# Kernel optimization log

Hardware: AMD Instinct MI355X
Metric: run time of the kernel (lower is better)

Reference implementation:

```python
import jax, jax.numpy as jnp
import numpy as np

EPS = 1e-6


def _expand_mask(mask, D, H, W):
    # mask: (B,1,f,f,f) bool -> (B,1,D,H,W) via repeat_interleave on each spatial axis
    m = jnp.repeat(mask, D // mask.shape[2], axis=2)
    m = jnp.repeat(m, H // mask.shape[3], axis=3)
    m = jnp.repeat(m, W // mask.shape[4], axis=4)
    return m


def setup_inputs() -> dict:
    key = jax.random.key(0)
    ks = jax.random.split(key, 10)
    B, C, D, H, W = 2, 192, 32, 32, 32
    K, HID = 7, 4 * C
    x = jax.random.normal(ks[0], (B, C, D, H, W), dtype=jnp.float32)
    mask = jax.random.randint(ks[1], (B, 1, 8, 8, 8), 0, 2) > 0
    dw_w = jax.random.normal(ks[2], (C, 1, K, K, K), dtype=jnp.float32) * (1.0 / np.sqrt(K**3))
    dw_b = jnp.zeros((C,), dtype=jnp.float32)
    ln_w = jnp.ones((C,), dtype=jnp.float32)
    ln_b = jnp.zeros((C,), dtype=jnp.float32)
    w1 = jax.random.normal(ks[3], (C, HID), dtype=jnp.float32) * (1.0 / np.sqrt(C))
    b1 = jnp.zeros((HID,), dtype=jnp.float32)
    w2 = jax.random.normal(ks[4], (HID, C), dtype=jnp.float32) * (1.0 / np.sqrt(HID))
    b2 = jnp.zeros((C,), dtype=jnp.float32)
    gamma = jnp.full((C,), 1e-6, dtype=jnp.float32)
    return {"x": x, "mask": mask, "dw_w": dw_w, "dw_b": dw_b, "ln_w": ln_w,
            "ln_b": ln_b, "w1": w1, "b1": b1, "w2": w2, "b2": b2, "gamma": gamma}


def reference(x, mask, dw_w, dw_b, ln_w, ln_b, w1, b1, w2, b2, gamma):
    B, C, D, H, W = x.shape
    m = _expand_mask(mask, D, H, W)              # (B,1,D,H,W) bool
    mf = m.astype(x.dtype)

    # depthwise 3D conv, SAME padding (padding = kernel//2), groups = C
    y = jax.lax.conv_general_dilated(
        x, dw_w, window_strides=(1, 1, 1), padding='SAME',
        dimension_numbers=('NCDHW', 'OIDHW', 'NCDHW'),
        feature_group_count=C)
    y = y + dw_b[None, :, None, None, None]

    # channels_last: (B,D,H,W,C)
    y = jnp.transpose(y, (0, 2, 3, 4, 1))

    # sparse LayerNorm over channel dim: normalize all tokens, keep only active
    # (equivalent to gather->LN->scatter-into-zeros in the original)
    mu = jnp.mean(y, axis=-1, keepdims=True)
    var = jnp.mean(jnp.square(y - mu), axis=-1, keepdims=True)
    ln = (y - mu) * jax.lax.rsqrt(var + EPS) * ln_w + ln_b
    ln = ln * jnp.transpose(mf, (0, 2, 3, 4, 1))  # zero inactive tokens

    # pointwise MLP
    h = jax.nn.gelu(jnp.einsum('bdhwc,ce->bdhwe', ln, w1) + b1, approximate=False)
    o = jnp.einsum('bdhwe,ec->bdhwc', h, w2) + b2
    o = gamma * o

    # back to channels_first and final sparse mask
    o = jnp.transpose(o, (0, 4, 1, 2, 3)) * mf
    return o
```

## Files before the change

kernel.cpp:

```cpp
#include <hip/hip_runtime.h>
#include <hip/hip_bf16.h>

typedef __attribute__((ext_vector_type(2))) float f2v;
typedef __attribute__((ext_vector_type(4))) float f4v;
typedef __attribute__((ext_vector_type(8))) short bf8v;
typedef __attribute__((ext_vector_type(8))) _Float16 h8v;

#define NPOS 32768
#define CCH  192
#define HID  768

#define WS_Y    ((size_t)0)
#define WS_B1F  ((size_t)25165824)
#define WS_B2F  ((size_t)25460736)
#define WS_WPF  ((size_t)25755648)
#define WS_B3F  ((size_t)26056704)
#define WS_TOTAL_MFMA ((size_t)35690496)
#define WS_TOTAL_DOT2 ((size_t)26056704)

__device__ inline unsigned short f2bf(float f){
  unsigned int u = __float_as_uint(f);
  u += 0x7FFFu + ((u >> 16) & 1u);
  return (unsigned short)(u >> 16);
}
__device__ inline float bf2f(unsigned short s){
  return __uint_as_float(((unsigned int)s) << 16);
}
__device__ inline float gelu_f(float x){
  float u = 0.7978845608028654f * x * fmaf(0.044715f, x*x, 1.0f);
  float e = __expf(2.0f*u);
  float th = __fdividef(e - 1.0f, e + 1.0f);
  return 0.5f*x*(1.0f + th);
}

#define DOT2(A, X, W) \
  asm("v_dot2_f32_f16 %0, %1, %2, %0" : "+v"(A) : "v"(X), "s"(W))

#define ZSTR 712
__global__ __launch_bounds__(256) void conv_mfma_kernel(
    const float* __restrict__ x, const float* __restrict__ dw_b,
    const unsigned short* __restrict__ b3f, unsigned short* __restrict__ yc)
{
  __shared__ unsigned short tile[22*ZSTR];

  int bid = blockIdx.x;
  int c = bid % 192;
  int r = bid / 192;
  int xq = r & 1, yq = (r >> 1) & 1, zh = (r >> 2) & 1, b = r >> 3;
  int tx0 = xq*16, ty0 = yq*16, zb = zh*16;

  int tid = threadIdx.x;
  const float* xsrc = x + ((size_t)(b*CCH + c))*NPOS;

  #pragma unroll
  for (int it = 0; it < 8; ++it) {
    int idx = tid + 256*it;
    if (idx < 1936) {
      int ci = idx & 3;
      int row = idx >> 2;
      int lz = row / 22, ly = row - lz*22;
      int gz = zb - 3 + lz, gy = ty0 - 3 + ly;
      f4v v0 = {0.f,0.f,0.f,0.f}, v1 = {0.f,0.f,0.f,0.f};
      if (((unsigned)gz < 32u) & ((unsigned)gy < 32u) & (ci < 3)) {
        int gx0 = tx0 - 4 + 8*ci;
        const float* src = xsrc + (size_t)gz*1024 + gy*32;
        if ((unsigned)gx0 <= 28u)     v0 = *(const f4v*)(src + gx0);
        if ((unsigned)(gx0+4) <= 28u) v1 = *(const f4v*)(src + gx0 + 4);
      }
      h8v pk;
      pk[0] = (_Float16)v0[0]; pk[1] = (_Float16)v0[1];
      pk[2] = (_Float16)v0[2]; pk[3] = (_Float16)v0[3];
      pk[4] = (_Float16)v1[0]; pk[5] = (_Float16)v1[1];
      pk[6] = (_Float16)v1[2]; pk[7] = (_Float16)v1[3];
      *(h8v*)(tile + lz*ZSTR + ly*32 + ci*8) = pk;
    }
  }
  __syncthreads();

  int wv = tid >> 6, lane = tid & 63;
  int q = lane >> 4, zm = lane & 15;

  const unsigned short* abase = tile + (size_t)zm*ZSTR + q*8;
  const unsigned short* bbase = b3f + ((size_t)c*49)*512 + (size_t)lane*8;

  f4v acc[4];
  #pragma unroll
  for (int t = 0; t < 4; ++t) acc[t] = (f4v){0.f,0.f,0.f,0.f};

  h8v Bc = *(const h8v*)(bbase);
  #pragma unroll 1
  for (int kz = 0; kz < 7; ++kz) {
    h8v Af[10];
    #pragma unroll
    for (int rr = 0; rr < 10; ++rr)
      Af[rr] = *(const h8v*)(abase + kz*ZSTR + (4*wv + rr)*32);
    #pragma unroll
    for (int ky = 0; ky < 7; ++ky) {
      int tap = kz*7 + ky;
      int tnx = (tap < 48) ? tap + 1 : 48;
      h8v Bn = *(const h8v*)(bbase + (size_t)tnx*512);
      acc[0] = __builtin_amdgcn_mfma_f32_16x16x32_f16(Af[ky+0], Bc, acc[0], 0, 0, 0);
      acc[1] = __builtin_amdgcn_mfma_f32_16x16x32_f16(Af[ky+1], Bc, acc[1], 0, 0, 0);
      acc[2] = __builtin_amdgcn_mfma_f32_16x16x32_f16(Af[ky+2], Bc, acc[2], 0, 0, 0);
      acc[3] = __builtin_amdgcn_mfma_f32_16x16x32_f16(Af[ky+3], Bc, acc[3], 0, 0, 0);
      Bc = Bn;
    }
  }

  float bias = dw_b[c];
  int cz = zh*4 + q;
  int cx = (tx0 >> 2) + (zm >> 2);
  int xr = zm & 3;
  int cy = (ty0 >> 2) + wv;
  int cell = cz*64 + cy*8 + cx;
  unsigned short* yb0 = yc + (((size_t)(b*512 + cell))*192 + c)*64 + xr;
  #pragma unroll
  for (int t = 0; t < 4; ++t) {
    unsigned short* yb = yb0 + t*4;
    yb[0]  = f2bf(acc[t][0] + bias);
    yb[16] = f2bf(acc[t][1] + bias);
    yb[32] = f2bf(acc[t][2] + bias);
    yb[48] = f2bf(acc[t][3] + bias);
  }
}

__global__ __launch_bounds__(256, 6) void conv_dw_f16_kernel(
    const float* __restrict__ x, const float* __restrict__ dw_b,
    const unsigned int* __restrict__ wpf, unsigned short* __restrict__ yc)
{
  __shared__ unsigned short ring[22*528];

  int bid = blockIdx.x;
  int c = bid % 192;
  int r = bid / 192;
  int xq = r & 1, yq = (r >> 1) & 1, zh = (r >> 2) & 1, b = r >> 3;
  int tx0 = xq*16, ty0 = yq*16, zb = zh*16;

  int tid = threadIdx.x;
  const float* xsrc = x + ((size_t)(b*CCH + c))*NPOS;

  for (int idx = tid; idx < 2904; idx += 256) {
    int sl = idx / 132;
    int rem = idx - sl*132;
    int rr = rem / 6, ci = rem - rr*6;
    int zi = zb - 3 + sl, gy = ty0 - 3 + rr, gx = tx0 - 4 + 4*ci;
    f4v v = {0.f, 0.f, 0.f, 0.f};
    if ((unsigned)zi < 32u && (unsigned)gy < 32u && (unsigned)gx <= 28u)
      v = *(const f4v*)(xsrc + (size_t)zi*1024 + gy*32 + gx);
    union { _Float16 h[4]; uint2 u2; } pk;
    pk.h[0] = (_Float16)v[0]; pk.h[1] = (_Float16)v[1];
    pk.h[2] = (_Float16)v[2]; pk.h[3] = (_Float16)v[3];
    *(uint2*)(ring + sl*528 + rr*24 + ci*4) = pk.u2;
  }
  __syncthreads();

  int p = tid & 15, zl = tid >> 4;
  int px = p & 3, py = p >> 2;
  int y0 = py*4, px4 = px*4;
  const unsigned short* base = ring + zl*528 + y0*24 + px4;
  const unsigned int* wb = wpf + (size_t)c*392;

  float acc[4][4];
  #pragma unroll
  for (int i = 0; i < 4; ++i)
    #pragma unroll
    for (int j = 0; j < 4; ++j) acc[i][j] = 0.f;

  #pragma unroll 1
  for (int s = 0; s < 7; ++s) {
    const unsigned short* sb = base + s*528;
    const unsigned int* wrow = wb + s*56;
    #pragma unroll
    for (int rr = 0; rr < 10; ++rr) {
      const unsigned short* rb = sb + rr*24;
      uint2 q0 = *(const uint2*)(rb);
      uint2 q1 = *(const uint2*)(rb + 4);
      uint2 q2 = *(const uint2*)(rb + 8);
      unsigned int D[6] = {q0.x, q0.y, q1.x, q1.y, q2.x, q2.y};
      #pragma unroll
      for (int dy = 0; dy < 4; ++dy) {
        int ky = rr - dy;
        if (ky < 0 || ky > 6) continue;
        const unsigned int* wk = wrow + ky*8;
        #pragma unroll
        for (int t = 0; t < 4; ++t) {
          DOT2(acc[dy][0], D[t],   wk[t]);
          DOT2(acc[dy][1], D[t+1], wk[4+t]);
          DOT2(acc[dy][2], D[t+1], wk[t]);
          DOT2(acc[dy][3], D[t+2], wk[4+t]);
        }
      }
    }
  }

  float bias = dw_b[c];
  int z = zb + zl;
  int cz = z >> 2, cx = (tx0 >> 2) + px, cy = (ty0 >> 2) + py;
  int cell = cz*64 + cy*8 + cx;
  unsigned short* ybase = yc + (((size_t)(b*512 + cell))*192 + c)*64;
  int tokz = (z & 3)*16;
  #pragma unroll
  for (int dy = 0; dy < 4; ++dy) {
    ushort4 o;
    o.x = f2bf(acc[dy][0] + bias);
    o.y = f2bf(acc[dy][1] + bias);
    o.z = f2bf(acc[dy][2] + bias);
    o.w = f2bf(acc[dy][3] + bias);
    *(ushort4*)(ybase + tokz + dy*4) = o;
  }
}

__global__ __launch_bounds__(256) void conv_dw_f32_kernel(
    const float* __restrict__ x, const float* __restrict__ dw_w,
    const float* __restrict__ dw_b, unsigned short* __restrict__ yc)
{
  __shared__ float ring[22*528];

  int bid = blockIdx.x;
  int c = bid % 192;
  int r = bid / 192;
  int xq = r & 1, yq = (r >> 1) & 1, zh = (r >> 2) & 1, b = r >> 3;
  int tx0 = xq*16, ty0 = yq*16, zb = zh*16;

  int tid = threadIdx.x;
  const float* xsrc = x + ((size_t)(b*CCH + c))*NPOS;

  for (int idx = tid; idx < 2904; idx += 256) {
    int sl = idx / 132;
    int rem = idx - sl*132;
    int rr = rem / 6, ci = rem - rr*6;
    int zi = zb - 3 + sl, gy = ty0 - 3 + rr, gx = tx0 - 4 + 4*ci;
    f4v v = {0.f, 0.f, 0.f, 0.f};
    if ((unsigned)zi < 32u && (unsigned)gy < 32u && (unsigned)gx <= 28u)
      v = *(const f4v*)(xsrc + (size_t)zi*1024 + gy*32 + gx);
    *(f4v*)(ring + sl*528 + rr*24 + ci*4) = v;
  }
  __syncthreads();

  int p = tid & 15, zl = tid >> 4;
  int px = p & 3, py = p >> 2;
  int y0 = py*4, px4 = px*4;
  const float* base = ring + zl*528 + y0*24 + px4;
  const float* wbase = dw_w + (size_t)c*343;

  f2v acc[8];
  #pragma unroll
  for (int i = 0; i < 8; ++i) acc[i] = (f2v){0.f, 0.f};

  #pragma unroll 1
  for (int s = 0; s < 7; ++s) {
    const float* sb = base + s*528;
    f4v n0 = *(const f4v*)(sb);
    f4v n1 = *(const f4v*)(sb + 4);
    f4v n2 = *(const f4v*)(sb + 8);
    #pragma unroll
    for (int rr = 0; rr < 10; ++rr) {
      f4v r0 = n0, r1 = n1, r2 = n2;
      if (rr < 9) {
        n0 = *(const f4v*)(sb + (rr+1)*24);
        n1 = *(const f4v*)(sb + (rr+1)*24 + 4);
        n2 = *(const f4v*)(sb + (rr+1)*24 + 8);
      }
      f2v pr[10];
      pr[1] = (f2v){r0[1], r0[2]};
      pr[2] = (f2v){r0[2], r0[3]};
      pr[3] = (f2v){r0[3], r1[0]};
      pr[4] = (f2v){r1[0], r1[1]};
      pr[5] = (f2v){r1[1], r1[2]};
      pr[6] = (f2v){r1[2], r1[3]};
      pr[7] = (f2v){r1[3], r2[0]};
      pr[8] = (f2v){r2[0], r2[1]};
      pr[9] = (f2v){r2[1], r2[2]};
      #pragma unroll
      for (int dy = 0; dy < 4; ++dy) {
        int ky = rr - dy;
        if (ky < 0 || ky > 6) continue;
        #pragma unroll
        for (int kx = 0; kx < 7; ++kx) {
          float w = wbase[s*49 + ky*7 + kx];
          f2v wv = (f2v){w, w};
          acc[dy*2+0] = __builtin_elementwise_fma(wv, pr[kx+1], acc[dy*2+0]);
          acc[dy*2+1] = __builtin_elementwise_fma(wv, pr[kx+3], acc[dy*2+1]);
        }
      }
    }
  }

  float bias = dw_b[c];
  int z = zb + zl;
  int cz = z >> 2, cx = (tx0 >> 2) + px, cy = (ty0 >> 2) + py;
  int cell = cz*64 + cy*8 + cx;
  unsigned short* ybase = yc + (((size_t)(b*512 + cell))*192 + c)*64;
  int tokz = (z & 3)*16;
  #pragma unroll
  for (int dy = 0; dy < 4; ++dy) {
    ushort4 o;
    o.x = f2bf(acc[dy*2+0][0] + bias);
    o.y = f2bf(acc[dy*2+0][1] + bias);
    o.z = f2bf(acc[dy*2+1][0] + bias);
    o.w = f2bf(acc[dy*2+1][1] + bias);
    *(ushort4*)(ybase + tokz + dy*4) = o;
  }
}

__global__ __launch_bounds__(256) void prep_w_kernel(
    const float* __restrict__ w1, const float* __restrict__ w2,
    const float* __restrict__ dw_w,
    unsigned short* __restrict__ b1f, unsigned short* __restrict__ b2f,
    unsigned int* __restrict__ wpf, unsigned short* __restrict__ b3f)
{
  int gid = blockIdx.x*256 + threadIdx.x;
  if (gid < 18432) {
    int fi = gid;
    int lane = fi & 63, fr = fi >> 6;
    int nt = fr / 6, ks = fr - nt*6;
    int n  = nt*16 + (lane & 15);
    int kb = ks*32 + (lane >> 4)*8;
    #pragma unroll
    for (int j = 0; j < 8; ++j) b1f[fi*8 + j] = f2bf(w1[(kb+j)*HID + n]);
  } else if (gid < 36864) {
    int fi = gid - 18432;
    int lane = fi & 63, fr = fi >> 6;
    int nt = fr / 24, ks = fr - nt*24;
    int n  = nt*16 + (lane & 15);
    int kb = ks*32 + (lane >> 4)*8;
    #pragma unroll
    for (int j = 0; j < 8; ++j) b2f[fi*8 + j] = f2bf(w2[(kb+j)*CCH + n]);
  } else if (gid < 46272) {
    int ci = gid - 36864;
    int cch = ci / 49, t7 = ci - cch*49;
    const float* wr = dw_w + cch*343 + t7*7;
    float w[8];
    #pragma unroll
    for (int j = 0; j < 7; ++j) w[j] = wr[j];
    w[7] = 0.f;
    union { _Float16 h[2]; unsigned int u; } pk;
    #pragma unroll
    for (int t = 0; t < 4; ++t) {
      pk.h[0] = (t == 0) ? (_Float16)0.f : (_Float16)w[2*t-1];
      pk.h[1] = (_Float16)w[2*t];
      wpf[ci*8 + t] = pk.u;
    }
    #pragma unroll
    for (int t = 0; t < 4; ++t) {
      pk.h[0] = (_Float16)w[2*t];
      pk.h[1] = (_Float16)w[2*t+1];
      wpf[ci*8 + 4 + t] = pk.u;
    }
  } else if (gid < 648384) {
    int fi = gid - 46272;
    int lane = fi & 63, frag = fi >> 6;
    int cch = frag / 49, tap = frag - cch*49;
    const float* wr = dw_w + cch*343 + tap*7;
    int q = lane >> 4, n = lane & 15;
    h8v pk;
    #pragma unroll
    for (int j = 0; j < 8; ++j) {
      int t = q*8 + j - n - 1;
      pk[j] = (t >= 0 && t <= 6) ? (_Float16)wr[t] : (_Float16)0.f;
    }
    *(h8v*)(b3f + (size_t)fi*8) = pk;
  }
}

__global__ __launch_bounds__(256) void mlp_kernel(
    const unsigned short* __restrict__ yc, const unsigned short* __restrict__ b1f,
    const unsigned short* __restrict__ b2f, const float* __restrict__ b1,
    const float* __restrict__ b2, const float* __restrict__ gamma,
    const float* __restrict__ ln_w, const float* __restrict__ ln_b,
    const int* __restrict__ mask, float* __restrict__ out)
{
  int bid = blockIdx.x;
  int b = bid >> 9, cell = bid & 511;
  int cz = cell >> 6, cy = (cell >> 3) & 7, cx = cell & 7;
  int z0 = cz*4, y0 = cy*4, x0 = cx*4;
  int tid = threadIdx.x, wave = tid >> 6, lane = tid & 63;
  int lq = lane >> 4, ln15 = lane & 15;

  if (mask[bid] == 0) {
    f4v z4 = {0.f, 0.f, 0.f, 0.f};
    #pragma unroll
    for (int pp = 0; pp < 12; ++pp) {
      int i4 = tid + 256*pp;
      int c = i4 >> 4, rem = i4 & 15;
      int dz = rem >> 2, dy = rem & 3;
      *(f4v*)(out + ((size_t)(b*CCH + c))*NPOS
                  + (size_t)(z0+dz)*1024 + (y0+dy)*32 + x0) = z4;
    }
    return;
  }

  __shared__ __align__(16) char uni[26112];
  unsigned short* ymat = (unsigned short*)uni;
  unsigned short* hbuf = (unsigned short*)uni;
  __shared__ unsigned short aFrag[12288];
  __shared__ float sred[2][4][64];
  __shared__ float murs[2][64];

  const unsigned short* ysrc = yc + (size_t)bid*12288;

  #pragma unroll
  for (int k = 0; k < 12; ++k) {
    int idx = tid + 256*k;
    int c = idx >> 4, t4 = idx & 15;
    *(ushort4*)(ymat + c*68 + t4*4) = *(const ushort4*)(ysrc + c*64 + t4*4);
  }
  __syncthreads();

  {
    int tok = tid & 63, part = tid >> 6;
    float S = 0.f, Q = 0.f;
    #pragma unroll
    for (int j = 0; j < 48; ++j) {
      float v = bf2f(ymat[(part*48 + j)*68 + tok]);
      S += v; Q = fmaf(v, v, Q);
    }
    sred[0][part][tok] = S; sred[1][part][tok] = Q;
  }
  __syncthreads();
  if (tid < 64) {
    float S = sred[0][0][tid] + sred[0][1][tid] + sred[0][2][tid] + sred[0][3][tid];
    float Q = sred[1][0][tid] + sred[1][1][tid] + sred[1][2][tid] + sred[1][3][tid];
    float m = S*(1.f/192.f);
    float var = Q*(1.f/192.f) - m*m;
    murs[0][tid] = m;
    murs[1][tid] = rsqrtf(var + 1e-6f);
  }
  __syncthreads();

  #pragma unroll
  for (int k = 0; k < 6; ++k) {
    int fi = tid + 256*k;
    int lane2 = fi & 63, rest = fi >> 6;
    int mt = rest / 6, ks = rest - mt*6;
    int tok = mt*16 + (lane2 & 15);
    int cc0 = ks*32 + (lane2 >> 4)*8;
    float m = murs[0][tok], rs = murs[1][tok];
    f4v lw0 = *(const f4v*)(ln_w + cc0), lw1 = *(const f4v*)(ln_w + cc0 + 4);
    f4v lb0 = *(const f4v*)(ln_b + cc0), lb1 = *(const f4v*)(ln_b + cc0 + 4);
    union { bf8v v; unsigned short u[8]; } pk;
    #pragma unroll
    for (int j = 0; j < 4; ++j) {
      float v0 = (bf2f(ymat[(cc0+j)*68 + tok])   - m)*rs*lw0[j] + lb0[j];
      float v1 = (bf2f(ymat[(cc0+4+j)*68 + tok]) - m)*rs*lw1[j] + lb1[j];
      pk.u[j] = f2bf(v0); pk.u[4+j] = f2bf(v1);
    }
    *(bf8v*)(aFrag + fi*8) = pk.v;
  }
  __syncthreads();

  f4v acc2[4][3];
  #pragma unroll
  for (int mt = 0; mt < 4; ++mt)
    #pragma unroll
    for (int nt = 0; nt < 3; ++nt)
      acc2[mt][nt] = (f4v){0.f, 0.f, 0.f, 0.f};

  const unsigned short* p1base = b1f + wave*2*3072 + lane*8;
  const unsigned short* p2base = b2f + wave*3*12288 + lane*8;

  bf8v B1r[12];
  #pragma unroll
  for (int i = 0; i < 12; ++i) {
    int jj = i / 6, ks = i - jj*6;
    B1r[i] = *(const bf8v*)(p1base + jj*3072 + ks*512);
  }

  #pragma unroll 1
  for (int ch = 0; ch < 6; ++ch) {
    bf8v B2r[12];
    const unsigned short* p2 = p2base + ch*2048;
    #pragma unroll
    for (int ks2 = 0; ks2 < 4; ++ks2)
      #pragma unroll
      for (int nt = 0; nt < 3; ++nt)
        B2r[ks2*3 + nt] = *(const bf8v*)(p2 + nt*12288 + ks2*512);

    f4v a1[2][4];
    #pragma unroll
    for (int jj = 0; jj < 2; ++jj)
      #pragma unroll
      for (int mt = 0; mt < 4; ++mt) a1[jj][mt] = (f4v){0.f,0.f,0.f,0.f};
    #pragma unroll
    for (int ks = 0; ks < 6; ++ks) {
      bf8v Af[4];
      #pragma unroll
      for (int mt = 0; mt < 4; ++mt)
        Af[mt] = *(const bf8v*)(aFrag + ((mt*6 + ks)*64 + lane)*8);
      #pragma unroll
      for (int jj = 0; jj < 2; ++jj)
        #pragma unroll
        for (int mt = 0; mt < 4; ++mt)
          a1[jj][mt] = __builtin_amdgcn_mfma_f32_16x16x32_bf16(Af[mt], B1r[jj*6+ks], a1[jj][mt], 0, 0, 0);
    }

    if (ch < 5) {
      const unsigned short* p1 = p1base + (ch+1)*24576;
      #pragma unroll
      for (int i = 0; i < 12; ++i) {
        int jj = i / 6, ks = i - jj*6;
        B1r[i] = *(const bf8v*)(p1 + jj*3072 + ks*512);
      }
    }

    #pragma unroll
    for (int jj = 0; jj < 2; ++jj) {
      float b1v = b1[(ch*8 + wave*2 + jj)*16 + ln15];
      int lane_hi = jj*2 + (ln15 >> 3);
      #pragma unroll
      for (int mt = 0; mt < 4; ++mt)
        #pragma unroll
        for (int rr = 0; rr < 4; ++rr) {
          float g = gelu_f(a1[jj][mt][rr] + b1v);
          int elem = ((mt*4 + wave)*64 + lane_hi*16 + (lq*4 + rr))*8 + (lane & 7);
          hbuf[elem] = f2bf(g);
        }
    }
    __syncthreads();
    #pragma unroll
    for (int ks2 = 0; ks2 < 4; ++ks2) {
      bf8v A2[4];
      #pragma unroll
      for (int mt = 0; mt < 4; ++mt)
        A2[mt] = *(const bf8v*)(hbuf + ((mt*4 + ks2)*64 + lane)*8);
      #pragma unroll
      for (int nt = 0; nt < 3; ++nt)
        #pragma unroll
        for (int mt = 0; mt < 4; ++mt)
          acc2[mt][nt] = __builtin_amdgcn_mfma_f32_16x16x32_bf16(A2[mt], B2r[ks2*3+nt], acc2[mt][nt], 0, 0, 0);
    }
    __syncthreads();
  }

  #pragma unroll
  for (int nt = 0; nt < 3; ++nt) {
    int c = (wave*3 + nt)*16 + ln15;
    float gm = gamma[c], bb = b2[c];
    size_t cbase = ((size_t)(b*CCH + c))*NPOS + (size_t)(y0 + lq)*32 + x0;
    #pragma unroll
    for (int mt = 0; mt < 4; ++mt) {
      f4v o;
      o[0] = gm*(acc2[mt][nt][0] + bb);
      o[1] = gm*(acc2[mt][nt][1] + bb);
      o[2] = gm*(acc2[mt][nt][2] + bb);
      o[3] = gm*(acc2[mt][nt][3] + bb);
      *(f4v*)(out + cbase + (size_t)(z0 + mt)*1024) = o;
    }
  }
}

extern "C" void kernel_launch(void* const* d_in, const int* in_sizes, int n_in,
                              void* d_out, int out_size, void* d_ws, size_t ws_size,
                              hipStream_t stream) {
  const float* x     = (const float*)d_in[0];
  const int*   mask  = (const int*)  d_in[1];
  const float* dw_w  = (const float*)d_in[2];
  const float* dw_b  = (const float*)d_in[3];
  const float* ln_w  = (const float*)d_in[4];
  const float* ln_b  = (const float*)d_in[5];
  const float* w1    = (const float*)d_in[6];
  const float* b1    = (const float*)d_in[7];
  const float* w2    = (const float*)d_in[8];
  const float* b2    = (const float*)d_in[9];
  const float* gamma = (const float*)d_in[10];
  float* out = (float*)d_out;
  char* ws = (char*)d_ws;

  unsigned short* yc  = (unsigned short*)(ws + WS_Y);
  unsigned short* b1f = (unsigned short*)(ws + WS_B1F);
  unsigned short* b2f = (unsigned short*)(ws + WS_B2F);
  unsigned int*   wpf = (unsigned int*)(ws + WS_WPF);
  unsigned short* b3f = (unsigned short*)(ws + WS_B3F);

  bool mfma_ok = ws_size >= WS_TOTAL_MFMA;
  bool dot2_ok = ws_size >= WS_TOTAL_DOT2;
  int prep_grid = mfma_ok ? 2533 : (dot2_ok ? 181 : 144);
  prep_w_kernel<<<prep_grid, 256, 0, stream>>>(w1, w2, dw_w, b1f, b2f, wpf, b3f);
  if (mfma_ok)
    conv_mfma_kernel<<<3072, 256, 0, stream>>>(x, dw_b, b3f, yc);
  else if (dot2_ok)
    conv_dw_f16_kernel<<<3072, 256, 0, stream>>>(x, dw_b, wpf, yc);
  else
    conv_dw_f32_kernel<<<3072, 256, 0, stream>>>(x, dw_w, dw_b, yc);
  mlp_kernel<<<1024, 256, 0, stream>>>(yc, b1f, b2f, b1, b2, gamma, ln_w, ln_b, mask, out);
}
```

Measured before the change: 238.8 us.

## Compact active cells into a list so MLP blocks schedule active work first

```diff
diff --git a/kernel.cpp b/kernel.cpp
--- a/kernel.cpp
+++ b/kernel.cpp
@@ -35,6 +35,34 @@
 
 #define DOT2(A, X, W) \
   asm("v_dot2_f32_f16 %0, %1, %2, %0" : "+v"(A) : "v"(X), "s"(W))
+
+__global__ __launch_bounds__(256) void compact_kernel(
+    const int* __restrict__ mask, int* __restrict__ list)
+{
+  __shared__ unsigned short cnt[256];
+  __shared__ int pref[257];
+  int t = threadIdx.x;
+  int m[4], c0 = 0;
+  #pragma unroll
+  for (int i = 0; i < 4; ++i) { m[i] = mask[t*4 + i]; c0 += (m[i] != 0); }
+  cnt[t] = (unsigned short)c0;
+  __syncthreads();
+  if (t == 0) {
+    int s = 0;
+    for (int i = 0; i < 256; ++i) { pref[i] = s; s += cnt[i]; }
+    pref[256] = s;
+  }
+  __syncthreads();
+  int na = pref[256];
+  int pa = pref[t];
+  int pi = na + (t*4 - pref[t]);
+  #pragma unroll
+  for (int i = 0; i < 4; ++i) {
+    if (m[i]) list[pa++] = t*4 + i;
+    else      list[pi++] = t*4 + i;
+  }
+  if (t == 0) list[1024] = na;
+}
 
 #define ZSTR 712
 __global__ __launch_bounds__(256) void conv_mfma_kernel(
@@ -87,23 +115,22 @@
   #pragma unroll
   for (int t = 0; t < 4; ++t) acc[t] = (f4v){0.f,0.f,0.f,0.f};
 
-  h8v Bc = *(const h8v*)(bbase);
   #pragma unroll 1
   for (int kz = 0; kz < 7; ++kz) {
+    h8v Bt[7];
+    #pragma unroll
+    for (int ky = 0; ky < 7; ++ky)
+      Bt[ky] = *(const h8v*)(bbase + (size_t)(kz*7 + ky)*512);
     h8v Af[10];
     #pragma unroll
     for (int rr = 0; rr < 10; ++rr)
       Af[rr] = *(const h8v*)(abase + kz*ZSTR + (4*wv + rr)*32);
     #pragma unroll
     for (int ky = 0; ky < 7; ++ky) {
-      int tap = kz*7 + ky;
-      int tnx = (tap < 48) ? tap + 1 : 48;
-      h8v Bn = *(const h8v*)(bbase + (size_t)tnx*512);
-      acc[0] = __builtin_amdgcn_mfma_f32_16x16x32_f16(Af[ky+0], Bc, acc[0], 0, 0, 0);
-      acc[1] = __builtin_amdgcn_mfma_f32_16x16x32_f16(Af[ky+1], Bc, acc[1], 0, 0, 0);
-      acc[2] = __builtin_amdgcn_mfma_f32_16x16x32_f16(Af[ky+2], Bc, acc[2], 0, 0, 0);
-      acc[3] = __builtin_amdgcn_mfma_f32_16x16x32_f16(Af[ky+3], Bc, acc[3], 0, 0, 0);
-      Bc = Bn;
+      acc[0] = __builtin_amdgcn_mfma_f32_16x16x32_f16(Af[ky+0], Bt[ky], acc[0], 0, 0, 0);
+      acc[1] = __builtin_amdgcn_mfma_f32_16x16x32_f16(Af[ky+1], Bt[ky], acc[1], 0, 0, 0);
+      acc[2] = __builtin_amdgcn_mfma_f32_16x16x32_f16(Af[ky+2], Bt[ky], acc[2], 0, 0, 0);
+      acc[3] = __builtin_amdgcn_mfma_f32_16x16x32_f16(Af[ky+3], Bt[ky], acc[3], 0, 0, 0);
     }
   }
 
@@ -363,21 +390,32 @@
   }
 }
 
+template<int COMPACT>
 __global__ __launch_bounds__(256) void mlp_kernel(
     const unsigned short* __restrict__ yc, const unsigned short* __restrict__ b1f,
     const unsigned short* __restrict__ b2f, const float* __restrict__ b1,
     const float* __restrict__ b2, const float* __restrict__ gamma,
     const float* __restrict__ ln_w, const float* __restrict__ ln_b,
-    const int* __restrict__ mask, float* __restrict__ out)
+    const int* __restrict__ mask, const int* __restrict__ list,
+    float* __restrict__ out)
 {
   int bid = blockIdx.x;
-  int b = bid >> 9, cell = bid & 511;
+  int cid, active;
+  if constexpr (COMPACT) {
+    int na = list[1024];
+    cid = list[bid];
+    active = bid < na;
+  } else {
+    cid = bid;
+    active = (mask[bid] != 0);
+  }
+  int b = cid >> 9, cell = cid & 511;
   int cz = cell >> 6, cy = (cell >> 3) & 7, cx = cell & 7;
   int z0 = cz*4, y0 = cy*4, x0 = cx*4;
   int tid = threadIdx.x, wave = tid >> 6, lane = tid & 63;
   int lq = lane >> 4, ln15 = lane & 15;
 
-  if (mask[bid] == 0) {
+  if (!active) {
     f4v z4 = {0.f, 0.f, 0.f, 0.f};
     #pragma unroll
     for (int pp = 0; pp < 12; ++pp) {
@@ -397,7 +435,7 @@
   __shared__ float sred[2][4][64];
   __shared__ float murs[2][64];
 
-  const unsigned short* ysrc = yc + (size_t)bid*12288;
+  const unsigned short* ysrc = yc + (size_t)cid*12288;
 
   #pragma unroll
   for (int k = 0; k < 12; ++k) {
@@ -571,16 +609,21 @@
   unsigned short* b2f = (unsigned short*)(ws + WS_B2F);
   unsigned int*   wpf = (unsigned int*)(ws + WS_WPF);
   unsigned short* b3f = (unsigned short*)(ws + WS_B3F);
+  int*            lst = (int*)(ws + WS_WPF);
 
   bool mfma_ok = ws_size >= WS_TOTAL_MFMA;
   bool dot2_ok = ws_size >= WS_TOTAL_DOT2;
   int prep_grid = mfma_ok ? 2533 : (dot2_ok ? 181 : 144);
   prep_w_kernel<<<prep_grid, 256, 0, stream>>>(w1, w2, dw_w, b1f, b2f, wpf, b3f);
-  if (mfma_ok)
+  if (mfma_ok) {
+    compact_kernel<<<1, 256, 0, stream>>>(mask, lst);
     conv_mfma_kernel<<<3072, 256, 0, stream>>>(x, dw_b, b3f, yc);
-  else if (dot2_ok)
+    mlp_kernel<1><<<1024, 256, 0, stream>>>(yc, b1f, b2f, b1, b2, gamma, ln_w, ln_b, mask, lst, out);
+  } else if (dot2_ok) {
     conv_dw_f16_kernel<<<3072, 256, 0, stream>>>(x, dw_b, wpf, yc);
-  else
+    mlp_kernel<0><<<1024, 256, 0, stream>>>(yc, b1f, b2f, b1, b2, gamma, ln_w, ln_b, mask, nullptr, out);
+  } else {
     conv_dw_f32_kernel<<<3072, 256, 0, stream>>>(x, dw_w, dw_b, yc);
-  mlp_kernel<<<1024, 256, 0, stream>>>(yc, b1f, b2f, b1, b2, gamma, ln_w, ln_b, mask, out);
-}
+    mlp_kernel<0><<<1024, 256, 0, stream>>>(yc, b1f, b2f, b1, b2, gamma, ln_w, ln_b, mask, nullptr, out);
+  }
+}
```

New measurement: 227.0 us. 1.05x faster.
